# Kernel optimization log

Measured on AMD Instinct MI355X. Metric: run time of the kernel, lower is better.

## Reference

```python
import jax, jax.numpy as jnp
import numpy as np

# Init kwargs of DecisionGate
A = 1.0
B = 2.0
THRES = 0.5


def soft_gate(x):
    # 1 / (1 + |x/a|^(2b))
    return 1.0 / (1.0 + jnp.abs(x / A) ** (2.0 * B))


def setup_inputs() -> dict:
    key = jax.random.key(0)
    k1, k2 = jax.random.split(key)
    B_, P_, D_ = 4096, 64, 512
    x = jax.random.normal(k1, (B_, P_), dtype=jnp.float32)
    act = jax.random.normal(k2, (B_, D_), dtype=jnp.float32)
    batch_inds = jnp.arange(B_, dtype=jnp.int64)
    return {"x": x, "act": act, "batch_inds": batch_inds}


def reference(x, act, batch_inds):
    """Faithful dense formulation of DecisionGate.forward.

    The torch module returns (gated_x, dict{node p -> (list of act[b]*g[b,p], list of batch_inds[b])
    for all (b,p) with g[b,p] >= thres}). The variable-length dict is a sparse
    repacking of the dense dispatch tensor below: for node p, its gathered
    activations are dispatched[mask[:, p], p, :] and its batch ids are
    batch_inds[mask[:, p]]. We return (gated_x, mask, dispatched) as the
    fixed-shape, jit-compatible equivalent.
    """
    g = soft_gate(x)                      # [B, P]
    mask = g >= THRES                     # [B, P] bool routing decision
    w = jnp.where(mask, g, 0.0)           # zero out sub-threshold gates
    # dispatched[b, p, :] = act[b] * g[b, p] if routed to node p else 0
    dispatched = w[:, :, None] * act[:, None, :]  # [B, P, D]
    return g, mask, dispatched
```

## Files before the change

### kernel.cpp

```cpp
#include <hip/hip_runtime.h>


constexpr int BATCH = 4096;
constexpr int P = 64;
constexpr int D = 512;

typedef float vfloat4 __attribute__((ext_vector_type(4)));

__global__ __launch_bounds__(128)
void decision_gate_kernel(const float* __restrict__ x,
                          const float* __restrict__ act,
                          float* __restrict__ g_out,
                          float* __restrict__ mask_out,
                          float* __restrict__ disp) {
    __shared__ float w[P];

    const int b = blockIdx.x;
    const int t = threadIdx.x;

    if (t < P) {
        const float xv = x[(size_t)b * P + t];
        const float x2 = xv * xv;
        const float x4 = x2 * x2;
        const float g  = 1.0f / (1.0f + x4);
        const bool  m  = (g >= 0.5f);
        g_out[(size_t)b * P + t]    = g;
        mask_out[(size_t)b * P + t] = m ? 1.0f : 0.0f;
        w[t] = m ? g : 0.0f;
    }
    __syncthreads();

    const vfloat4 a = reinterpret_cast<const vfloat4*>(act)[(size_t)b * (D / 4) + t];

    vfloat4* out = reinterpret_cast<vfloat4*>(disp) + (size_t)b * (P * D / 4) + t;

    #pragma unroll 8
    for (int p = 0; p < P; ++p) {
        const float wp = w[p];
        vfloat4 v = a * wp;
        __builtin_nontemporal_store(v, out + (size_t)p * (D / 4));
    }
}

extern "C" void kernel_launch(void* const* d_in, const int* in_sizes, int n_in,
                              void* d_out, int out_size, void* d_ws, size_t ws_size,
                              hipStream_t stream) {
    const float* x   = (const float*)d_in[0];
    const float* act = (const float*)d_in[1];

    float* out      = (float*)d_out;
    float* g_out    = out;
    float* mask_out = out + (size_t)BATCH * P;
    float* disp     = out + (size_t)2 * BATCH * P;

    decision_gate_kernel<<<BATCH, 128, 0, stream>>>(x, act, g_out, mask_out, disp);
}
```

Measured before the change: 538.4 us.

## Split each batch row across eight blocks by gate chunk, recompute gates per thread

Each batch row is split across eight blocks that each handle eight gate columns, with 256 threads writing four float4 rows each. The shared-memory weight array and barrier go away; each thread recomputes its gate values from x directly. This gives more blocks and memory parallelism for the write-bound dispatch output. Stores change from nontemporal to regular, which could change cache behaviour on the large output write.

```diff
diff --git a/kernel.cpp b/kernel.cpp
--- a/kernel.cpp
+++ b/kernel.cpp
@@ -4,41 +4,49 @@
 constexpr int BATCH = 4096;
 constexpr int P = 64;
 constexpr int D = 512;
+constexpr int PCHUNK = 8;
+constexpr int NCHUNK = P / PCHUNK;
 
 typedef float vfloat4 __attribute__((ext_vector_type(4)));
 
-__global__ __launch_bounds__(128)
+__device__ __forceinline__ float gate_val(float xv) {
+    const float x2 = xv * xv;
+    const float x4 = x2 * x2;
+    return 1.0f / (1.0f + x4);
+}
+
+__global__ __launch_bounds__(256, 8)
 void decision_gate_kernel(const float* __restrict__ x,
                           const float* __restrict__ act,
                           float* __restrict__ g_out,
                           float* __restrict__ mask_out,
                           float* __restrict__ disp) {
-    __shared__ float w[P];
+    const int bid  = blockIdx.x;
+    const int b    = bid >> 3;
+    const int p0   = (bid & (NCHUNK - 1)) * PCHUNK;
+    const int t    = threadIdx.x;
+    const int d4   = t & 127;
+    const int psel = t >> 7;
 
-    const int b = blockIdx.x;
-    const int t = threadIdx.x;
+    if (t < PCHUNK) {
+        const float g = gate_val(x[(size_t)b * P + p0 + t]);
+        g_out[(size_t)b * P + p0 + t]    = g;
+        mask_out[(size_t)b * P + p0 + t] = (g >= 0.5f) ? 1.0f : 0.0f;
+    }
 
-    if (t < P) {
-        const float xv = x[(size_t)b * P + t];
-        const float x2 = xv * xv;
-        const float x4 = x2 * x2;
-        const float g  = 1.0f / (1.0f + x4);
-        const bool  m  = (g >= 0.5f);
-        g_out[(size_t)b * P + t]    = g;
-        mask_out[(size_t)b * P + t] = m ? 1.0f : 0.0f;
-        w[t] = m ? g : 0.0f;
-    }
-    __syncthreads();
+    const vfloat4 a = reinterpret_cast<const vfloat4*>(act)[(size_t)b * (D / 4) + d4];
 
-    const vfloat4 a = reinterpret_cast<const vfloat4*>(act)[(size_t)b * (D / 4) + t];
+    vfloat4* out = reinterpret_cast<vfloat4*>(disp)
+                 + (size_t)b * (P * D / 4)
+                 + (size_t)p0 * (D / 4)
+                 + d4;
 
-    vfloat4* out = reinterpret_cast<vfloat4*>(disp) + (size_t)b * (P * D / 4) + t;
-
-    #pragma unroll 8
-    for (int p = 0; p < P; ++p) {
-        const float wp = w[p];
-        vfloat4 v = a * wp;
-        __builtin_nontemporal_store(v, out + (size_t)p * (D / 4));
+    #pragma unroll
+    for (int k = 0; k < 4; ++k) {
+        const int p = psel + 2 * k;
+        const float g  = gate_val(x[(size_t)b * P + p0 + p]);
+        const float wp = (g >= 0.5f) ? g : 0.0f;
+        out[(size_t)p * (D / 4)] = a * wp;
     }
 }
 
@@ -53,5 +61,5 @@
     float* mask_out = out + (size_t)BATCH * P;
     float* disp     = out + (size_t)2 * BATCH * P;
 
-    decision_gate_kernel<<<BATCH, 128, 0, stream>>>(x, act, g_out, mask_out, disp);
+    decision_gate_kernel<<<BATCH * NCHUNK, 256, 0, stream>>>(x, act, g_out, mask_out, disp);
 }
```

After: 530.1 us. About the same (-1.5%).

## Use persistent 256-block grid with double-buffered gate weights and plain stores

Applied to the files above, without the earlier changes.

Replaces the one-block-per-row launch with 256 persistent blocks of 256 threads, each looping over 16 batch rows. Each wave writes 16 of the 64 gate rows, with two vectors per lane. Gate weights go into a double-buffered shared array so one barrier per row is enough. The nontemporal stores are dropped in favour of ordinary stores, which may change cache write behaviour on a store-bound kernel. With 256 blocks on a part with many CUs, occupancy is low and latency hiding may suffer.

```diff
diff --git a/kernel.cpp b/kernel.cpp
--- a/kernel.cpp
+++ b/kernel.cpp
@@ -5,40 +5,55 @@
 constexpr int P = 64;
 constexpr int D = 512;
 
+constexpr int NTHR = 256;
+constexpr int NBLK = 256;
+constexpr int ROWS = BATCH / NBLK;
+
 typedef float vfloat4 __attribute__((ext_vector_type(4)));
 
-__global__ __launch_bounds__(128)
+__device__ __forceinline__ float gate_val(float xv) {
+    const float x2 = xv * xv;
+    const float x4 = x2 * x2;
+    return 1.0f / (1.0f + x4);
+}
+
+__global__ __launch_bounds__(NTHR, 1)
 void decision_gate_kernel(const float* __restrict__ x,
                           const float* __restrict__ act,
                           float* __restrict__ g_out,
                           float* __restrict__ mask_out,
                           float* __restrict__ disp) {
-    __shared__ float w[P];
+    __shared__ float wbuf[2][P];
 
-    const int b = blockIdx.x;
-    const int t = threadIdx.x;
+    const int t    = threadIdx.x;
+    const int wave = t >> 6;
+    const int lane = t & 63;
 
-    if (t < P) {
-        const float xv = x[(size_t)b * P + t];
-        const float x2 = xv * xv;
-        const float x4 = x2 * x2;
-        const float g  = 1.0f / (1.0f + x4);
-        const bool  m  = (g >= 0.5f);
-        g_out[(size_t)b * P + t]    = g;
-        mask_out[(size_t)b * P + t] = m ? 1.0f : 0.0f;
-        w[t] = m ? g : 0.0f;
-    }
-    __syncthreads();
+    const vfloat4* __restrict__ actv = reinterpret_cast<const vfloat4*>(act);
+    vfloat4* __restrict__ dispv      = reinterpret_cast<vfloat4*>(disp);
 
-    const vfloat4 a = reinterpret_cast<const vfloat4*>(act)[(size_t)b * (D / 4) + t];
+    for (int k = 0; k < ROWS; ++k) {
+        const int b = blockIdx.x + NBLK * k;
 
-    vfloat4* out = reinterpret_cast<vfloat4*>(disp) + (size_t)b * (P * D / 4) + t;
+        const vfloat4 a0 = actv[(size_t)b * (D / 4) + lane];
+        const vfloat4 a1 = actv[(size_t)b * (D / 4) + 64 + lane];
 
-    #pragma unroll 8
-    for (int p = 0; p < P; ++p) {
-        const float wp = w[p];
-        vfloat4 v = a * wp;
-        __builtin_nontemporal_store(v, out + (size_t)p * (D / 4));
+        if (t < P) {
+            const float g = gate_val(x[(size_t)b * P + t]);
+            g_out[(size_t)b * P + t]    = g;
+            mask_out[(size_t)b * P + t] = (g >= 0.5f) ? 1.0f : 0.0f;
+            wbuf[k & 1][t] = (g >= 0.5f) ? g : 0.0f;
+        }
+        __syncthreads();
+
+        vfloat4* out = dispv + (size_t)b * (P * D / 4);
+        #pragma unroll
+        for (int i = 0; i < 16; ++i) {
+            const int p = 16 * wave + i;
+            const float wp = wbuf[k & 1][p];
+            out[(size_t)p * (D / 4) + lane]      = a0 * wp;
+            out[(size_t)p * (D / 4) + 64 + lane] = a1 * wp;
+        }
     }
 }
 
@@ -53,5 +68,5 @@
     float* mask_out = out + (size_t)BATCH * P;
     float* disp     = out + (size_t)2 * BATCH * P;
 
-    decision_gate_kernel<<<BATCH, 128, 0, stream>>>(x, act, g_out, mask_out, disp);
+    decision_gate_kernel<<<NBLK, NTHR, 0, stream>>>(x, act, g_out, mask_out, disp);
 }
```

Result: faster. 521.4 us (-3.2%).
